# Kernel tuning notes

Measured on AMD Instinct MI355X. Metric: run time of the kernel, lower is better.

The kernel has to match this reference:

```python
import jax, jax.numpy as jnp
import numpy as np

MAX_NEIGHBORS = 64  # static cap; >> observed max (~50) for n=9225 uniform pts, r=0.03


def setup_inputs() -> dict:
    key = jax.random.key(0)
    k1, k2 = jax.random.split(key)
    n_batch, n, m, d = 8, 9225, 4096, 2
    data = jax.random.uniform(k1, (n_batch, n, d), dtype=jnp.float32)
    queries = jax.random.uniform(k2, (n_batch, m, d), dtype=jnp.float32)
    radius = jnp.float32(0.03)
    return {"data": data, "queries": queries, "radius": radius}


def reference(data, queries, radius):
    # Faithful JAX translation of native_neighbor_search (use_open3d=False),
    # computed in one shot instead of q_chunk loops (same math), with a static
    # neighbor cap MAX_NEIGHBORS standing in for the data-dependent max.
    B, n, d = data.shape
    m = queries.shape[1]
    # Squared Euclidean distances via the GEMM expansion (equiv. to cdist<=r).
    qn = jnp.sum(queries * queries, axis=-1)              # [B, m]
    dn = jnp.sum(data * data, axis=-1)                    # [B, n]
    cross = jnp.einsum("bmd,bnd->bmn", queries, data)    # [B, m, n]
    sqd = jnp.maximum(qn[:, :, None] + dn[:, None, :] - 2.0 * cross, 0.0)
    in_nbr = sqd <= radius * radius                       # [B, m, n] bool
    counts = jnp.sum(in_nbr, axis=2).astype(jnp.int32)    # [B, m]
    idx = jnp.arange(n, dtype=jnp.int32)                  # [n]
    # invalid slots -> sentinel n, sort compacts valid indices to the front
    valid = jnp.where(in_nbr, idx[None, None, :], jnp.int32(n))
    sorted_idx = jnp.sort(valid, axis=2)[:, :, :MAX_NEIGHBORS]
    neighbors_index = jnp.where(sorted_idx == n, jnp.int32(-1), sorted_idx)
    neighbors_row_splits = jnp.concatenate(
        [jnp.zeros((B, 1), dtype=jnp.int32), jnp.cumsum(counts, axis=1)], axis=1
    )
    return neighbors_index, neighbors_row_splits
```

## Files before the change

kernel.cpp:

```cpp
#include <hip/hip_runtime.h>

#define BATCH 8
#define NPTS 9225
#define MQ 4096
#define CAP 64
#define GRID 64
#define NCELLS (GRID * GRID)

__device__ __forceinline__ int cell_of(float x, float y) {
  int cx = (int)(x * (float)GRID);
  int cy = (int)(y * (float)GRID);
  cx = min(max(cx, 0), GRID - 1);
  cy = min(max(cy, 0), GRID - 1);
  return cy * GRID + cx;
}

__global__ __launch_bounds__(1024) void build_kernel(
    const float* __restrict__ data,
    int* __restrict__ cell_starts,
    float4* __restrict__ recs) {
  __shared__ int hist[NCELLS];
  __shared__ int cursor[NCELLS];
  __shared__ int wavesum[16];
  const int b = blockIdx.x;
  const int t = threadIdx.x;
#pragma unroll
  for (int k = 0; k < NCELLS / 1024; ++k) hist[t + k * 1024] = 0;
  __syncthreads();

  const float2* dp = (const float2*)data + (size_t)b * NPTS;
  for (int i = t; i < NPTS; i += 1024)
    atomicAdd(&hist[cell_of(dp[i].x, dp[i].y)], 1);
  __syncthreads();

  const int c0 = hist[4 * t + 0], c1 = hist[4 * t + 1];
  const int c2 = hist[4 * t + 2], c3 = hist[4 * t + 3];
  const int s = c0 + c1 + c2 + c3;
  const int lane = t & 63, wid = t >> 6;
  int v = s;
#pragma unroll
  for (int off = 1; off < 64; off <<= 1) {
    const int u = __shfl_up(v, off, 64);
    if (lane >= off) v += u;
  }
  if (lane == 63) wavesum[wid] = v;
  __syncthreads();
  int woff = 0;
  for (int k = 0; k < wid; ++k) woff += wavesum[k];
  int e = woff + v - s;
  int* cs = cell_starts + b * (NCELLS + 1);
  cs[4 * t + 0] = e; cursor[4 * t + 0] = e; e += c0;
  cs[4 * t + 1] = e; cursor[4 * t + 1] = e; e += c1;
  cs[4 * t + 2] = e; cursor[4 * t + 2] = e; e += c2;
  cs[4 * t + 3] = e; cursor[4 * t + 3] = e; e += c3;
  if (t == 1023) cs[NCELLS] = e;
  __syncthreads();

  float4* rb = recs + (size_t)b * NPTS;
  for (int i = t; i < NPTS; i += 1024) {
    const float2 p = dp[i];
    const int pos = atomicAdd(&cursor[cell_of(p.x, p.y)], 1);
    rb[pos] = make_float4(p.x, p.y, __int_as_float(i), 0.0f);
  }
}

__global__ __launch_bounds__(256) void search_kernel(
    const float* __restrict__ queries, const float* __restrict__ radius_p,
    const int* __restrict__ cell_starts, const float4* __restrict__ recs,
    int* __restrict__ nbr_idx, int* __restrict__ counts) {
#pragma clang fp contract(off)
  __shared__ int hitbuf[4][CAP];
  const int lane = threadIdx.x & 63;
  const int w = threadIdx.x >> 6;
  const int q = blockIdx.x * 4 + w;
  const int b = q >> 12;
  const float r = radius_p[0];
  const float r2 = r * r;
  const float2 qv = ((const float2*)queries)[q];
  const float qx = qv.x, qy = qv.y;
  const float qn = qx * qx + qy * qy;

  const int cx = min(max((int)(qx * (float)GRID), 0), GRID - 1);
  const int cy = min(max((int)(qy * (float)GRID), 0), GRID - 1);
  const int x0 = max(cx - 2, 0), x1 = min(cx + 2, GRID - 1);
  const int y0 = max(cy - 2, 0), y1 = min(cy + 2, GRID - 1);

  const int csbase = b * (NCELLS + 1);
  int rstart[5], rlen[5];
  int nr = 0;
  for (int y = y0; y <= y1; ++y) {
    const int s0 = cell_starts[csbase + y * GRID + x0];
    const int s1 = cell_starts[csbase + y * GRID + x1 + 1];
    rstart[nr] = s0;
    rlen[nr] = s1 - s0;
    ++nr;
  }
  for (int k = nr; k < 5; ++k) { rstart[k] = 0; rlen[k] = 0; }
  const int L0 = rlen[0];
  const int L1 = L0 + rlen[1];
  const int L2 = L1 + rlen[2];
  const int L3 = L2 + rlen[3];
  const int T = L3 + rlen[4];

  const unsigned long long below = (1ull << lane) - 1ull;
  const float4* rb = recs + (size_t)b * NPTS;
  int h = 0;

  for (int base = 0; base < T; base += 64) {
    const int p = base + lane;
    const bool act = (p < T);
    int i;
    if (p < L0)      i = rstart[0] + p;
    else if (p < L1) i = rstart[1] + (p - L0);
    else if (p < L2) i = rstart[2] + (p - L1);
    else if (p < L3) i = rstart[3] + (p - L2);
    else             i = rstart[4] + (p - L3);
    if (!act) i = 0;
    const float4 rec = rb[i];
    const float dx = rec.x, dy = rec.y;
    const int id = __float_as_int(rec.z);
    const float dn = dx * dx + dy * dy;
    const float cross = qx * dx + qy * dy;
    const float s = (qn + dn) - 2.0f * cross;
    const bool in = act && (s <= r2);
    const unsigned long long mask = __ballot(in);
    if (in) {
      const int pos = h + __popcll(mask & below);
      if (pos < CAP) hitbuf[w][pos] = id;
    }
    h += __popcll(mask);
  }

  int v = (lane < h && lane < CAP) ? hitbuf[w][lane] : 0x7fffffff;

#pragma unroll
  for (int k = 2; k <= 32; k <<= 1) {
#pragma unroll
    for (int j = k >> 1; j >= 1; j >>= 1) {
      const int other = __shfl_xor(v, j, 64);
      const bool keep_min = (((lane & k) == 0) == ((lane & j) == 0));
      v = keep_min ? min(v, other) : max(v, other);
    }
  }
  if (h > 32) {
#pragma unroll
    for (int j = 32; j >= 1; j >>= 1) {
      const int other = __shfl_xor(v, j, 64);
      const bool keep_min = ((lane & j) == 0);
      v = keep_min ? min(v, other) : max(v, other);
    }
  }

  nbr_idx[(size_t)q * CAP + lane] = (v == 0x7fffffff) ? -1 : v;
  if (lane == 0) counts[q] = h;
}

__global__ __launch_bounds__(256) void scan_kernel(const int* __restrict__ counts,
                                                   int* __restrict__ row_splits) {
  const int b = blockIdx.x;
  const int t = threadIdx.x;
  const int PER = MQ / 256;
  __shared__ int partial[256];
  const int* c = counts + b * MQ;
  int local[PER];
  int sum = 0;
#pragma unroll
  for (int k = 0; k < PER; ++k) { local[k] = c[t * PER + k]; sum += local[k]; }
  partial[t] = sum;
  __syncthreads();
  for (int off = 1; off < 256; off <<= 1) {
    int u = (t >= off) ? partial[t - off] : 0;
    __syncthreads();
    partial[t] += u;
    __syncthreads();
  }
  const int excl = (t == 0) ? 0 : partial[t - 1];
  int* rs = row_splits + b * (MQ + 1);
  if (t == 0) rs[0] = 0;
  int run = excl;
#pragma unroll
  for (int k = 0; k < PER; ++k) { run += local[k]; rs[t * PER + k + 1] = run; }
}

extern "C" void kernel_launch(void* const* d_in, const int* in_sizes, int n_in,
                              void* d_out, int out_size, void* d_ws, size_t ws_size,
                              hipStream_t stream) {
  const float* data    = (const float*)d_in[0];
  const float* queries = (const float*)d_in[1];
  const float* radius  = (const float*)d_in[2];
  int* out        = (int*)d_out;
  int* nbr_idx    = out;
  int* row_splits = out + BATCH * MQ * CAP;

  int* counts      = (int*)d_ws;
  int* cell_starts = counts + BATCH * MQ;
  float4* recs     = (float4*)(cell_starts + BATCH * (NCELLS + 1));

  hipLaunchKernelGGL(build_kernel, dim3(BATCH), dim3(1024), 0, stream,
                     data, cell_starts, recs);
  hipLaunchKernelGGL(search_kernel, dim3(BATCH * MQ / 4), dim3(256), 0, stream,
                     queries, radius, cell_starts, recs, nbr_idx, counts);
  hipLaunchKernelGGL(scan_kernel, dim3(BATCH), dim3(256), 0, stream,
                     counts, row_splits);
}
```

Measured before the change: 91.09 us.

## Split grid build into multi-block histogram, scan, and scatter kernels

The single 8-block build kernel, which ran one 1024-thread block per batch using shared-memory histograms, is replaced by four kernels. A zero pass, a histogram pass with one thread per point using global atomics, a per-batch scan of the cell counts, and a scatter pass that also uses one thread per point. The aim is to spread the build across the whole GPU instead of 8 CUs, since the build stage was latency bound. In exchange it adds three kernel launches, global-memory atomic contention, and more workspace for the hist and cursor arrays.

```diff
diff --git a/kernel.cpp b/kernel.cpp
--- a/kernel.cpp
+++ b/kernel.cpp
@@ -6,6 +6,7 @@
 #define CAP 64
 #define GRID 64
 #define NCELLS (GRID * GRID)
+#define TOTPTS (BATCH * NPTS)
 
 __device__ __forceinline__ int cell_of(float x, float y) {
   int cx = (int)(x * (float)GRID);
@@ -15,26 +16,30 @@
   return cy * GRID + cx;
 }
 
-__global__ __launch_bounds__(1024) void build_kernel(
-    const float* __restrict__ data,
+
+__global__ __launch_bounds__(1024) void zero_hist_kernel(int* __restrict__ hist) {
+  hist[blockIdx.x * 1024 + threadIdx.x] = 0;
+}
+
+__global__ __launch_bounds__(256) void hist_kernel(
+    const float* __restrict__ data, int* __restrict__ hist) {
+  const int f = blockIdx.x * 256 + threadIdx.x;
+  if (f >= TOTPTS) return;
+  const float2 p = ((const float2*)data)[f];
+  const unsigned b = (unsigned)f / (unsigned)NPTS;
+  atomicAdd(&hist[b * NCELLS + cell_of(p.x, p.y)], 1);
+}
+
+__global__ __launch_bounds__(1024) void scan_cells_kernel(
+    const int* __restrict__ hist,
     int* __restrict__ cell_starts,
-    float4* __restrict__ recs) {
-  __shared__ int hist[NCELLS];
-  __shared__ int cursor[NCELLS];
+    int* __restrict__ cursor) {
   __shared__ int wavesum[16];
   const int b = blockIdx.x;
   const int t = threadIdx.x;
-#pragma unroll
-  for (int k = 0; k < NCELLS / 1024; ++k) hist[t + k * 1024] = 0;
-  __syncthreads();
-
-  const float2* dp = (const float2*)data + (size_t)b * NPTS;
-  for (int i = t; i < NPTS; i += 1024)
-    atomicAdd(&hist[cell_of(dp[i].x, dp[i].y)], 1);
-  __syncthreads();
-
-  const int c0 = hist[4 * t + 0], c1 = hist[4 * t + 1];
-  const int c2 = hist[4 * t + 2], c3 = hist[4 * t + 3];
+  const int* h = hist + b * NCELLS;
+  const int c0 = h[4 * t + 0], c1 = h[4 * t + 1];
+  const int c2 = h[4 * t + 2], c3 = h[4 * t + 3];
   const int s = c0 + c1 + c2 + c3;
   const int lane = t & 63, wid = t >> 6;
   int v = s;
@@ -49,19 +54,24 @@
   for (int k = 0; k < wid; ++k) woff += wavesum[k];
   int e = woff + v - s;
   int* cs = cell_starts + b * (NCELLS + 1);
-  cs[4 * t + 0] = e; cursor[4 * t + 0] = e; e += c0;
-  cs[4 * t + 1] = e; cursor[4 * t + 1] = e; e += c1;
-  cs[4 * t + 2] = e; cursor[4 * t + 2] = e; e += c2;
-  cs[4 * t + 3] = e; cursor[4 * t + 3] = e; e += c3;
+  int* cu = cursor + b * NCELLS;
+  cs[4 * t + 0] = e; cu[4 * t + 0] = e; e += c0;
+  cs[4 * t + 1] = e; cu[4 * t + 1] = e; e += c1;
+  cs[4 * t + 2] = e; cu[4 * t + 2] = e; e += c2;
+  cs[4 * t + 3] = e; cu[4 * t + 3] = e; e += c3;
   if (t == 1023) cs[NCELLS] = e;
-  __syncthreads();
-
-  float4* rb = recs + (size_t)b * NPTS;
-  for (int i = t; i < NPTS; i += 1024) {
-    const float2 p = dp[i];
-    const int pos = atomicAdd(&cursor[cell_of(p.x, p.y)], 1);
-    rb[pos] = make_float4(p.x, p.y, __int_as_float(i), 0.0f);
-  }
+}
+
+__global__ __launch_bounds__(256) void scatter_kernel(
+    const float* __restrict__ data, int* __restrict__ cursor,
+    float4* __restrict__ recs) {
+  const int f = blockIdx.x * 256 + threadIdx.x;
+  if (f >= TOTPTS) return;
+  const float2 p = ((const float2*)data)[f];
+  const unsigned b = (unsigned)f / (unsigned)NPTS;
+  const int i = f - (int)b * NPTS;
+  const int pos = atomicAdd(&cursor[b * NCELLS + cell_of(p.x, p.y)], 1);
+  recs[(size_t)b * NPTS + pos] = make_float4(p.x, p.y, __int_as_float(i), 0.0f);
 }
 
 __global__ __launch_bounds__(256) void search_kernel(
@@ -194,10 +204,20 @@
 
   int* counts      = (int*)d_ws;
   int* cell_starts = counts + BATCH * MQ;
-  float4* recs     = (float4*)(cell_starts + BATCH * (NCELLS + 1));
-
-  hipLaunchKernelGGL(build_kernel, dim3(BATCH), dim3(1024), 0, stream,
-                     data, cell_starts, recs);
+  int* hist        = cell_starts + BATCH * (NCELLS + 1);
+  int* cursor      = hist + BATCH * NCELLS;
+  float4* recs     = (float4*)(cursor + BATCH * NCELLS);
+
+  const int PT_BLOCKS = (TOTPTS + 255) / 256;
+
+  hipLaunchKernelGGL(zero_hist_kernel, dim3(BATCH * NCELLS / 1024), dim3(1024),
+                     0, stream, hist);
+  hipLaunchKernelGGL(hist_kernel, dim3(PT_BLOCKS), dim3(256), 0, stream,
+                     data, hist);
+  hipLaunchKernelGGL(scan_cells_kernel, dim3(BATCH), dim3(1024), 0, stream,
+                     hist, cell_starts, cursor);
+  hipLaunchKernelGGL(scatter_kernel, dim3(PT_BLOCKS), dim3(256), 0, stream,
+                     data, cursor, recs);
   hipLaunchKernelGGL(search_kernel, dim3(BATCH * MQ / 4), dim3(256), 0, stream,
                      queries, radius, cell_starts, recs, nbr_idx, counts);
   hipLaunchKernelGGL(scan_kernel, dim3(BATCH), dim3(256), 0, stream,
```

New measurement: 91.64 us. About the same (+0.6%).
